# Kernel tuning notes

Measured on AMD Instinct MI355X. Metric: run time of the kernel, lower is better.

The kernel has to match this reference:

```python
import jax, jax.numpy as jnp
import numpy as np

N_POS = 8
POS_W = jnp.array([0.95, 0.9, 0.85, 0.5, 0.4, 0.2, 0.15, 0.05], dtype=jnp.float32)
EVENT_HORIZON = 0.1

L, D = 4096, 2048


def setup_inputs() -> dict:
    key = jax.random.key(0)
    ks = jax.random.split(key, 10)
    token_vecs = jax.random.normal(ks[0], (L, D), dtype=jnp.float32)
    pos_idx = jax.random.randint(ks[1], (L,), 0, 8)
    depth = jax.random.randint(ks[2], (L,), 0, 12)
    token_pos = jnp.arange(L, dtype=jnp.int64) if jax.config.jax_enable_x64 else jnp.arange(L, dtype=jnp.int32)
    slot_idx = jax.random.randint(ks[3], (L,), 0, 16)
    confidences = jax.random.uniform(ks[4], (L,), dtype=jnp.float32)
    sun_resonances = jax.random.uniform(ks[5], (L,), dtype=jnp.float32)
    # learned parameters (match torch init)
    G_micro = jnp.full((N_POS, N_POS), 0.1, dtype=jnp.float32)
    G_macro = jnp.array(0.5, dtype=jnp.float32)
    k_spring = jnp.full((N_POS,), 0.05, dtype=jnp.float32)
    temperature = jnp.array(1.0, dtype=jnp.float32)
    Wv_w = jax.random.normal(ks[6], (D, D), dtype=jnp.float32) * 0.02
    Wv_b = jnp.zeros((D,), dtype=jnp.float32)
    Wo_w = jax.random.normal(ks[7], (D, D), dtype=jnp.float32) * 0.02
    Wo_b = jnp.zeros((D,), dtype=jnp.float32)
    return dict(token_vecs=token_vecs, pos_idx=pos_idx, depth=depth,
                token_pos=token_pos, slot_idx=slot_idx, confidences=confidences,
                sun_resonances=sun_resonances, G_micro=G_micro, G_macro=G_macro,
                k_spring=k_spring, temperature=temperature, Wv_w=Wv_w, Wv_b=Wv_b,
                Wo_w=Wo_w, Wo_b=Wo_b)


def _scores(token_vecs, pos_idx, depth, token_pos, slot_idx, confidences,
            sun_resonances, G_micro, G_macro, k_spring):
    n = token_vecs.shape[0]
    p = pos_idx % N_POS
    # semantic mass: ||v|| detached in torch (.item()), POS weight, (1 + resonance)
    norms = jax.lax.stop_gradient(jnp.linalg.norm(token_vecs, axis=-1))
    res = jax.lax.stop_gradient(sun_resonances)
    conf = jax.lax.stop_gradient(confidences)
    m = norms * POS_W[p] * (1.0 + res)                     # [L]
    mm = m[:, None] * m[None, :]                            # [L, L]
    # micro gravity: per-POS-pair G over squared slot distance (min 1)
    slot_d = jnp.abs(slot_idx[:, None] - slot_idx[None, :])
    r_slot = jnp.maximum(slot_d, 1).astype(jnp.float32)
    f_micro = jax.nn.sigmoid(G_micro)[p[:, None], p[None, :]] * mm / (r_slot * r_slot)
    # macro gravity over orbital (depth) distance
    r_orb = (jnp.abs(depth[:, None] - depth[None, :]) + 1).astype(jnp.float32)
    f_macro = jax.nn.sigmoid(G_macro) * mm / (r_orb * r_orb)
    # spring force grows with token distance, k indexed by row POS
    tok_d = jnp.abs(token_pos[:, None] - token_pos[None, :]).astype(jnp.float32)
    f_spring = jax.nn.sigmoid(k_spring)[p][:, None] * tok_d
    # black hole force
    collapsed = conf <= EVENT_HORIZON
    gap = jnp.where(collapsed, 1.0, conf - EVENT_HORIZON)
    bh = jnp.where(collapsed, -1e6, -0.01 / (gap * gap))    # [L]
    total = f_micro + f_macro + f_spring + bh[:, None] + bh[None, :]
    eye = jnp.eye(n, dtype=bool)
    row_skip = (bh < -1e5)[:, None]                          # collapsed rows stay zero
    return jnp.where(row_skip | eye, 0.0, total)


def reference(token_vecs, pos_idx, depth, token_pos, slot_idx, confidences,
              sun_resonances, G_micro, G_macro, k_spring, temperature,
              Wv_w, Wv_b, Wo_w, Wo_b):
    scores = _scores(token_vecs, pos_idx, depth, token_pos, slot_idx,
                     confidences, sun_resonances, G_micro, G_macro, k_spring)
    T = jnp.maximum(jnp.abs(temperature), 0.1)
    A = jax.nn.softmax(scores / T, axis=-1)
    V = token_vecs @ Wv_w.T + Wv_b
    out = (A @ V) @ Wo_w.T + Wo_b
    return out, A, scores
```

## Files before the change

### kernel.cpp

```cpp
#include <hip/hip_runtime.h>
#include <math.h>

#define LL 4096
#define DD 2048

typedef __attribute__((ext_vector_type(8))) short short8;
typedef __attribute__((ext_vector_type(4))) float f32x4;
typedef unsigned int u32;
typedef unsigned short u16;

__device__ __constant__ float POS_W_c[8] = {0.95f, 0.9f, 0.85f, 0.5f, 0.4f, 0.2f, 0.15f, 0.05f};

static __device__ inline u32 f2bf(float f) {
    u32 u = __builtin_bit_cast(u32, f);
    return (u + 0x7fffu + ((u >> 16) & 1u)) >> 16;
}
static __device__ inline u32 cvt2_bf16(float a, float b) {
    return f2bf(a) | (f2bf(b) << 16);
}
static __device__ inline short8 pack8_bf16(float4 a, float4 b) {
    uint4 u = make_uint4(cvt2_bf16(a.x, a.y), cvt2_bf16(a.z, a.w),
                         cvt2_bf16(b.x, b.y), cvt2_bf16(b.z, b.w));
    return __builtin_bit_cast(short8, u);
}

__global__ __launch_bounds__(256) void row_stats_k(
    const float* __restrict__ tv, const int* __restrict__ pos_idx,
    const float* __restrict__ conf, const float* __restrict__ res,
    const float* __restrict__ k_spring,
    float* __restrict__ m_arr, float* __restrict__ bh_arr,
    float* __restrict__ spring_arr, int* __restrict__ coll_arr)
{
    int i = blockIdx.x;
    int t = threadIdx.x;
    const float4* row = (const float4*)(tv + (size_t)i * DD);
    float s = 0.0f;
#pragma unroll
    for (int c = 0; c < 2; ++c) {
        float4 v = row[t + c * 256];
        s += v.x * v.x + v.y * v.y + v.z * v.z + v.w * v.w;
    }
#pragma unroll
    for (int o = 32; o; o >>= 1) s += __shfl_xor(s, o);
    __shared__ float tmp[4];
    if ((t & 63) == 0) tmp[t >> 6] = s;
    __syncthreads();
    if (t == 0) {
        float tot = tmp[0] + tmp[1] + tmp[2] + tmp[3];
        float norm = sqrtf(tot);
        int p = pos_idx[i] & 7;
        float m = norm * POS_W_c[p] * (1.0f + res[i]);
        float cf = conf[i];
        bool col = (cf <= 0.1f);
        float gap = col ? 1.0f : (cf - 0.1f);
        float bh = col ? -1e6f : (-0.01f / (gap * gap));
        m_arr[i] = m;
        bh_arr[i] = bh;
        coll_arr[i] = (bh < -1e5f) ? 1 : 0;
        spring_arr[i] = 1.0f / (1.0f + __expf(-k_spring[p]));
    }
}

__global__ __launch_bounds__(256) void scores_k(
    const int* __restrict__ pos_idx, const int* __restrict__ depth,
    const int* __restrict__ token_pos, const int* __restrict__ slot_idx,
    const float* __restrict__ m_arr, const float* __restrict__ bh_arr,
    const float* __restrict__ spring_arr, const int* __restrict__ coll_arr,
    const float* __restrict__ G_micro, const float* __restrict__ G_macro,
    const float* __restrict__ temperature,
    float* __restrict__ scores, float* __restrict__ Amat)
{
    int i = blockIdx.x;
    int t = threadIdx.x;
    int lane = t & 63, wid = t >> 6;

    __shared__ float sigG[64];
    __shared__ float red[4];
    if (t < 64) sigG[t] = 1.0f / (1.0f + __expf(-G_micro[t]));
    __syncthreads();

    float sGmac = 1.0f / (1.0f + __expf(-G_macro[0]));
    float T = fmaxf(fabsf(temperature[0]), 0.1f);
    float invT = 1.0f / T;

    int pi = pos_idx[i] & 7;
    float mi = m_arr[i];
    float bhi = bh_arr[i];
    float spr = spring_arr[i];
    int sloti = slot_idx[i], depi = depth[i], tpi = token_pos[i];
    bool rowskip = (coll_arr[i] != 0);

    float* srow = scores + (size_t)i * LL;
    float* arow = Amat + (size_t)i * LL;

    float x[16];
    float xmax = -3.4e38f;
#pragma unroll
    for (int c = 0; c < 16; ++c) {
        int j = t + c * 256;
        float s = 0.0f;
        if (!rowskip && j != i) {
            float mj = m_arr[j];
            float mm = mi * mj;
            int pj = pos_idx[j] & 7;
            int sd = abs(sloti - slot_idx[j]); if (sd < 1) sd = 1;
            float rs = (float)sd;
            float fmic = sigG[pi * 8 + pj] * mm * __builtin_amdgcn_rcpf(rs * rs);
            int od = abs(depi - depth[j]) + 1;
            float ro = (float)od;
            float fmac = sGmac * mm * __builtin_amdgcn_rcpf(ro * ro);
            float td = fabsf((float)(tpi - token_pos[j]));
            s = fmic + fmac + spr * td + bhi + bh_arr[j];
        }
        srow[j] = s;
        x[c] = s * invT;
        xmax = fmaxf(xmax, x[c]);
    }
#pragma unroll
    for (int o = 32; o; o >>= 1) xmax = fmaxf(xmax, __shfl_xor(xmax, o));
    if (lane == 0) red[wid] = xmax;
    __syncthreads();
    xmax = fmaxf(fmaxf(red[0], red[1]), fmaxf(red[2], red[3]));
    __syncthreads();
    float e[16];
    float esum = 0.0f;
#pragma unroll
    for (int c = 0; c < 16; ++c) {
        e[c] = __expf(x[c] - xmax);
        esum += e[c];
    }
#pragma unroll
    for (int o = 32; o; o >>= 1) esum += __shfl_xor(esum, o);
    if (lane == 0) red[wid] = esum;
    __syncthreads();
    float inv = 1.0f / (red[0] + red[1] + red[2] + red[3]);
#pragma unroll
    for (int c = 0; c < 16; ++c) {
        arow[t + c * 256] = e[c] * inv;
    }
}

template <int A_BF16, int B_BF16, int BIAS, int OUT_BF16>
__global__ __launch_bounds__(256) void gemm_nt_k(
    const void* __restrict__ Ap, const void* __restrict__ Bp,
    const float* __restrict__ bias, void* __restrict__ Cp,
    int M, int N, int K)
{
    __shared__ __align__(16) short lA[4096];
    __shared__ __align__(16) short lB[4096];

    int t = threadIdx.x;
    int blockN = blockIdx.x * 128, blockM = blockIdx.y * 128;
    int wid = t >> 6, lane = t & 63;
    int wm = wid >> 1, wn = wid & 1;
    int r = lane & 15, bq = lane >> 4;

    f32x4 acc[4][4];
#pragma unroll
    for (int a = 0; a < 4; ++a)
#pragma unroll
        for (int b = 0; b < 4; ++b) acc[a][b] = (f32x4){0.f, 0.f, 0.f, 0.f};

    int m0 = t >> 2;
    int kb = t & 3;

    for (int kt = 0; kt < K; kt += 32) {
        short8 va0, va1, vb0, vb1;
        if (A_BF16) {
            const u16* A16 = (const u16*)Ap;
            va0 = *(const short8*)(A16 + (size_t)(blockM + m0) * K + kt + kb * 8);
            va1 = *(const short8*)(A16 + (size_t)(blockM + m0 + 64) * K + kt + kb * 8);
        } else {
            const float* Af = (const float*)Ap;
            const float4* p0 = (const float4*)(Af + (size_t)(blockM + m0) * K + kt + kb * 8);
            const float4* p1 = (const float4*)(Af + (size_t)(blockM + m0 + 64) * K + kt + kb * 8);
            float4 u0 = p0[0], u1 = p0[1];
            float4 u2 = p1[0], u3 = p1[1];
            va0 = pack8_bf16(u0, u1);
            va1 = pack8_bf16(u2, u3);
        }
        if (B_BF16) {
            const u16* B16 = (const u16*)Bp;
            vb0 = *(const short8*)(B16 + (size_t)(blockN + m0) * K + kt + kb * 8);
            vb1 = *(const short8*)(B16 + (size_t)(blockN + m0 + 64) * K + kt + kb * 8);
        } else {
            const float* Bf = (const float*)Bp;
            const float4* p0 = (const float4*)(Bf + (size_t)(blockN + m0) * K + kt + kb * 8);
            const float4* p1 = (const float4*)(Bf + (size_t)(blockN + m0 + 64) * K + kt + kb * 8);
            float4 u0 = p0[0], u1 = p0[1];
            float4 u2 = p1[0], u3 = p1[1];
            vb0 = pack8_bf16(u0, u1);
            vb1 = pack8_bf16(u2, u3);
        }
        __syncthreads();
        *(short8*)&lA[kb * 1024 + m0 * 8] = va0;
        *(short8*)&lA[kb * 1024 + (m0 + 64) * 8] = va1;
        *(short8*)&lB[kb * 1024 + m0 * 8] = vb0;
        *(short8*)&lB[kb * 1024 + (m0 + 64) * 8] = vb1;
        __syncthreads();

        short8 aF[4], bF[4];
#pragma unroll
        for (int mi = 0; mi < 4; ++mi)
            aF[mi] = *(const short8*)&lA[bq * 1024 + (wm * 64 + mi * 16 + r) * 8];
#pragma unroll
        for (int ni = 0; ni < 4; ++ni)
            bF[ni] = *(const short8*)&lB[bq * 1024 + (wn * 64 + ni * 16 + r) * 8];
#pragma unroll
        for (int mi = 0; mi < 4; ++mi)
#pragma unroll
            for (int ni = 0; ni < 4; ++ni)
                acc[mi][ni] = __builtin_amdgcn_mfma_f32_16x16x32_bf16(aF[mi], bF[ni], acc[mi][ni], 0, 0, 0);
    }

#pragma unroll
    for (int mi = 0; mi < 4; ++mi) {
        int rowb = blockM + wm * 64 + mi * 16 + bq * 4;
#pragma unroll
        for (int ni = 0; ni < 4; ++ni) {
            int col = blockN + wn * 64 + ni * 16 + r;
#pragma unroll
            for (int q = 0; q < 4; ++q) {
                float v = acc[mi][ni][q];
                int row = rowb + q;
                if (BIAS == 1) v += bias[row];
                else if (BIAS == 2) v += bias[col];
                if (OUT_BF16) {
                    ((u16*)Cp)[(size_t)row * N + col] = (u16)f2bf(v);
                } else {
                    ((float*)Cp)[(size_t)row * N + col] = v;
                }
            }
        }
    }
}

extern "C" void kernel_launch(void* const* d_in, const int* in_sizes, int n_in,
                              void* d_out, int out_size, void* d_ws, size_t ws_size,
                              hipStream_t stream) {
    (void)in_sizes; (void)n_in; (void)out_size; (void)ws_size;
    const float* tv        = (const float*)d_in[0];
    const int* pos_idx     = (const int*)d_in[1];
    const int* depth       = (const int*)d_in[2];
    const int* token_pos   = (const int*)d_in[3];
    const int* slot_idx    = (const int*)d_in[4];
    const float* conf      = (const float*)d_in[5];
    const float* res       = (const float*)d_in[6];
    const float* G_micro   = (const float*)d_in[7];
    const float* G_macro   = (const float*)d_in[8];
    const float* k_spring  = (const float*)d_in[9];
    const float* temperature = (const float*)d_in[10];
    const float* Wv_w      = (const float*)d_in[11];
    const float* Wv_b      = (const float*)d_in[12];
    const float* Wo_w      = (const float*)d_in[13];
    const float* Wo_b      = (const float*)d_in[14];

    float* out    = (float*)d_out;
    float* Amat   = out + (size_t)LL * DD;
    float* scores = Amat + (size_t)LL * LL;

    u16* VT = (u16*)d_ws;
    u16* H  = VT + (size_t)DD * LL;
    float* m_arr      = (float*)(H + (size_t)LL * DD);
    float* bh_arr     = m_arr + LL;
    float* spring_arr = bh_arr + LL;
    int*   coll_arr   = (int*)(spring_arr + LL);

    row_stats_k<<<LL, 256, 0, stream>>>(tv, pos_idx, conf, res, k_spring,
                                        m_arr, bh_arr, spring_arr, coll_arr);

    scores_k<<<LL, 256, 0, stream>>>(pos_idx, depth, token_pos, slot_idx,
                                     m_arr, bh_arr, spring_arr, coll_arr,
                                     G_micro, G_macro, temperature,
                                     scores, Amat);

    gemm_nt_k<0, 0, 1, 1><<<dim3(LL / 128, DD / 128), 256, 0, stream>>>(
        Wv_w, tv, Wv_b, VT, DD, LL, DD);

    gemm_nt_k<0, 1, 0, 1><<<dim3(DD / 128, LL / 128), 256, 0, stream>>>(
        Amat, VT, nullptr, H, LL, DD, LL);

    gemm_nt_k<1, 0, 2, 0><<<dim3(DD / 128, LL / 128), 256, 0, stream>>>(
        H, Wo_w, Wo_b, out, LL, DD, DD);
}
```

Before: 546.0 us.

## Pre-convert GEMM operands to bf16 and load tiles via global_load_lds

```diff
diff --git a/kernel.cpp b/kernel.cpp
--- a/kernel.cpp
+++ b/kernel.cpp
@@ -22,6 +22,23 @@
     uint4 u = make_uint4(cvt2_bf16(a.x, a.y), cvt2_bf16(a.z, a.w),
                          cvt2_bf16(b.x, b.y), cvt2_bf16(b.z, b.w));
     return __builtin_bit_cast(short8, u);
+}
+static __device__ inline void glds16(const u16* g, u16* l) {
+    __builtin_amdgcn_global_load_lds(
+        (const __attribute__((address_space(1))) void*)g,
+        (__attribute__((address_space(3))) void*)l, 16, 0, 0);
+}
+
+__global__ __launch_bounds__(256) void f32_to_bf16_k(
+    const float* __restrict__ in, u16* __restrict__ out, int n8)
+{
+    int idx = blockIdx.x * 256 + threadIdx.x;
+    int stride = gridDim.x * 256;
+    for (int i = idx; i < n8; i += stride) {
+        const float4* p = (const float4*)(in + (size_t)i * 8);
+        float4 a = p[0], b = p[1];
+        *(short8*)(out + (size_t)i * 8) = pack8_bf16(a, b);
+    }
 }
 
 __global__ __launch_bounds__(256) void row_stats_k(
@@ -68,7 +85,8 @@
     const float* __restrict__ spring_arr, const int* __restrict__ coll_arr,
     const float* __restrict__ G_micro, const float* __restrict__ G_macro,
     const float* __restrict__ temperature,
-    float* __restrict__ scores, float* __restrict__ Amat)
+    float* __restrict__ scores, float* __restrict__ Amat,
+    u16* __restrict__ Ab)
 {
     int i = blockIdx.x;
     int t = threadIdx.x;
@@ -92,6 +110,7 @@
 
     float* srow = scores + (size_t)i * LL;
     float* arow = Amat + (size_t)i * LL;
+    u16* abrow = Ab + (size_t)i * LL;
 
     float x[16];
     float xmax = -3.4e38f;
@@ -136,24 +155,26 @@
     float inv = 1.0f / (red[0] + red[1] + red[2] + red[3]);
 #pragma unroll
     for (int c = 0; c < 16; ++c) {
-        arow[t + c * 256] = e[c] * inv;
-    }
-}
-
-template <int A_BF16, int B_BF16, int BIAS, int OUT_BF16>
-__global__ __launch_bounds__(256) void gemm_nt_k(
-    const void* __restrict__ Ap, const void* __restrict__ Bp,
+        float a = e[c] * inv;
+        arow[t + c * 256] = a;
+        abrow[t + c * 256] = (u16)f2bf(a);
+    }
+}
+
+template <int BIAS, int OUT_BF16>
+__global__ __launch_bounds__(256) void gemm_bf16_k(
+    const u16* __restrict__ Ap, const u16* __restrict__ Bp,
     const float* __restrict__ bias, void* __restrict__ Cp,
     int M, int N, int K)
 {
-    __shared__ __align__(16) short lA[4096];
-    __shared__ __align__(16) short lB[4096];
+    __shared__ __align__(1024) u16 lA[4096];
+    __shared__ __align__(1024) u16 lB[4096];
 
     int t = threadIdx.x;
-    int blockN = blockIdx.x * 128, blockM = blockIdx.y * 128;
     int wid = t >> 6, lane = t & 63;
     int wm = wid >> 1, wn = wid & 1;
     int r = lane & 15, bq = lane >> 4;
+    int blockN = blockIdx.x * 128, blockM = blockIdx.y * 128;
 
     f32x4 acc[4][4];
 #pragma unroll
@@ -161,51 +182,27 @@
 #pragma unroll
         for (int b = 0; b < 4; ++b) acc[a][b] = (f32x4){0.f, 0.f, 0.f, 0.f};
 
-    int m0 = t >> 2;
-    int kb = t & 3;
+    int s0 = wid * 2, s1 = wid * 2 + 1;
+    const u16* gA0 = Ap + (size_t)(blockM + s0 * 16 + r) * K + bq * 8;
+    const u16* gA1 = Ap + (size_t)(blockM + s1 * 16 + r) * K + bq * 8;
+    const u16* gB0 = Bp + (size_t)(blockN + s0 * 16 + r) * K + bq * 8;
+    const u16* gB1 = Bp + (size_t)(blockN + s1 * 16 + r) * K + bq * 8;
 
     for (int kt = 0; kt < K; kt += 32) {
-        short8 va0, va1, vb0, vb1;
-        if (A_BF16) {
-            const u16* A16 = (const u16*)Ap;
-            va0 = *(const short8*)(A16 + (size_t)(blockM + m0) * K + kt + kb * 8);
-            va1 = *(const short8*)(A16 + (size_t)(blockM + m0 + 64) * K + kt + kb * 8);
-        } else {
-            const float* Af = (const float*)Ap;
-            const float4* p0 = (const float4*)(Af + (size_t)(blockM + m0) * K + kt + kb * 8);
-            const float4* p1 = (const float4*)(Af + (size_t)(blockM + m0 + 64) * K + kt + kb * 8);
-            float4 u0 = p0[0], u1 = p0[1];
-            float4 u2 = p1[0], u3 = p1[1];
-            va0 = pack8_bf16(u0, u1);
-            va1 = pack8_bf16(u2, u3);
-        }
-        if (B_BF16) {
-            const u16* B16 = (const u16*)Bp;
-            vb0 = *(const short8*)(B16 + (size_t)(blockN + m0) * K + kt + kb * 8);
-            vb1 = *(const short8*)(B16 + (size_t)(blockN + m0 + 64) * K + kt + kb * 8);
-        } else {
-            const float* Bf = (const float*)Bp;
-            const float4* p0 = (const float4*)(Bf + (size_t)(blockN + m0) * K + kt + kb * 8);
-            const float4* p1 = (const float4*)(Bf + (size_t)(blockN + m0 + 64) * K + kt + kb * 8);
-            float4 u0 = p0[0], u1 = p0[1];
-            float4 u2 = p1[0], u3 = p1[1];
-            vb0 = pack8_bf16(u0, u1);
-            vb1 = pack8_bf16(u2, u3);
-        }
         __syncthreads();
-        *(short8*)&lA[kb * 1024 + m0 * 8] = va0;
-        *(short8*)&lA[kb * 1024 + (m0 + 64) * 8] = va1;
-        *(short8*)&lB[kb * 1024 + m0 * 8] = vb0;
-        *(short8*)&lB[kb * 1024 + (m0 + 64) * 8] = vb1;
+        glds16(gA0 + kt, &lA[s0 * 512]);
+        glds16(gA1 + kt, &lA[s1 * 512]);
+        glds16(gB0 + kt, &lB[s0 * 512]);
+        glds16(gB1 + kt, &lB[s1 * 512]);
         __syncthreads();
 
         short8 aF[4], bF[4];
 #pragma unroll
         for (int mi = 0; mi < 4; ++mi)
-            aF[mi] = *(const short8*)&lA[bq * 1024 + (wm * 64 + mi * 16 + r) * 8];
+            aF[mi] = *(const short8*)&lA[(wm * 4 + mi) * 512 + lane * 8];
 #pragma unroll
         for (int ni = 0; ni < 4; ++ni)
-            bF[ni] = *(const short8*)&lB[bq * 1024 + (wn * 64 + ni * 16 + r) * 8];
+            bF[ni] = *(const short8*)&lB[(wn * 4 + ni) * 512 + lane * 8];
 #pragma unroll
         for (int mi = 0; mi < 4; ++mi)
 #pragma unroll
@@ -259,27 +256,36 @@
     float* Amat   = out + (size_t)LL * DD;
     float* scores = Amat + (size_t)LL * LL;
 
-    u16* VT = (u16*)d_ws;
-    u16* H  = VT + (size_t)DD * LL;
-    float* m_arr      = (float*)(H + (size_t)LL * DD);
+    u16* Ab = (u16*)out;
+
+    u16* VT  = (u16*)d_ws;
+    u16* H   = VT + (size_t)DD * LL;
+    u16* tvb = H + (size_t)LL * DD;
+    u16* Wvb = tvb + (size_t)LL * DD;
+    u16* Wob = Wvb + (size_t)DD * DD;
+    float* m_arr      = (float*)(Wob + (size_t)DD * DD);
     float* bh_arr     = m_arr + LL;
     float* spring_arr = bh_arr + LL;
     int*   coll_arr   = (int*)(spring_arr + LL);
 
+    f32_to_bf16_k<<<2048, 256, 0, stream>>>(tv, tvb, LL * DD / 8);
+    f32_to_bf16_k<<<1024, 256, 0, stream>>>(Wv_w, Wvb, DD * DD / 8);
+    f32_to_bf16_k<<<1024, 256, 0, stream>>>(Wo_w, Wob, DD * DD / 8);
+
     row_stats_k<<<LL, 256, 0, stream>>>(tv, pos_idx, conf, res, k_spring,
                                         m_arr, bh_arr, spring_arr, coll_arr);
 
     scores_k<<<LL, 256, 0, stream>>>(pos_idx, depth, token_pos, slot_idx,
                                      m_arr, bh_arr, spring_arr, coll_arr,
                                      G_micro, G_macro, temperature,
-                                     scores, Amat);
-
-    gemm_nt_k<0, 0, 1, 1><<<dim3(LL / 128, DD / 128), 256, 0, stream>>>(
-        Wv_w, tv, Wv_b, VT, DD, LL, DD);
-
-    gemm_nt_k<0, 1, 0, 1><<<dim3(DD / 128, LL / 128), 256, 0, stream>>>(
-        Amat, VT, nullptr, H, LL, DD, LL);
-
-    gemm_nt_k<1, 0, 2, 0><<<dim3(DD / 128, LL / 128), 256, 0, stream>>>(
-        H, Wo_w, Wo_b, out, LL, DD, DD);
-}
+                                     scores, Amat, Ab);
+
+    gemm_bf16_k<1, 1><<<dim3(LL / 128, DD / 128), 256, 0, stream>>>(
+        Wvb, tvb, Wv_b, VT, DD, LL, DD);
+
+    gemm_bf16_k<0, 1><<<dim3(DD / 128, LL / 128), 256, 0, stream>>>(
+        Ab, VT, nullptr, H, LL, DD, LL);
+
+    gemm_bf16_k<2, 0><<<dim3(DD / 128, LL / 128), 256, 0, stream>>>(
+        H, Wob, Wo_b, out, LL, DD, DD);
+}
```

New measurement: 536.7 us. Within noise of the previous version (-1.7%).
